# Performance work log

Measured on AMD Instinct MI355X. Metric: run time of the kernel, lower is better.

Reference implementation:

```python
import jax, jax.numpy as jnp
import numpy as np

B, S, H, NH = 2, 4096, 768, 12
DH = H // NH  # 64


def setup_inputs() -> dict:
    key = jax.random.key(0)
    ks = jax.random.split(key, 7)
    scale = 0.02
    return {
        "x": jax.random.normal(ks[0], (B, S, H), dtype=jnp.float32),
        "Wq": jax.random.normal(ks[1], (H, H), dtype=jnp.float32) * scale,
        "bq": jax.random.normal(ks[2], (H,), dtype=jnp.float32) * scale,
        "Wk": jax.random.normal(ks[3], (H, H), dtype=jnp.float32) * scale,
        "bk": jax.random.normal(ks[4], (H,), dtype=jnp.float32) * scale,
        "Wv": jax.random.normal(ks[5], (H, H), dtype=jnp.float32) * scale,
        "bv": jax.random.normal(ks[6], (H,), dtype=jnp.float32) * scale,
    }


def _split_heads(t):
    # [B,S,H] -> [B,NH,S,DH]
    return t.reshape(B, S, NH, DH).transpose(0, 2, 1, 3)


def reference(x, Wq, bq, Wk, bk, Wv, bv):
    q = _split_heads(x @ Wq + bq)
    k = _split_heads(x @ Wk + bk)
    v = _split_heads(x @ Wv + bv)
    # raw scores + zero additive mask (mask is all zeros, so it is a no-op)
    scores = jnp.einsum("bhqd,bhkd->bhqk", q, k) / jnp.sqrt(jnp.float32(DH))
    probs = jax.nn.softmax(scores, axis=-1)
    ctx = jnp.einsum("bhqk,bhkd->bhqd", probs, v)
    out = ctx.transpose(0, 2, 1, 3).reshape(B, S, H)
    return jnp.tanh(out)
```

## Files before the change

kernel.cpp:

```cpp
#include <hip/hip_runtime.h>
#include <hip/hip_bf16.h>

#define B_ 2
#define S_ 4096
#define H_ 768
#define NH_ 12
#define DH_ 64
#define M_ (B_ * S_)
#define N3_ (3 * H_)
#define NQK 1536
#define K_ H_
#define LOG2E 1.4426950408889634f

typedef __attribute__((ext_vector_type(8))) short short8;
typedef __attribute__((ext_vector_type(4))) float f32x4;
typedef __attribute__((ext_vector_type(16))) float f32x16;
typedef __attribute__((ext_vector_type(4))) unsigned int uint4v;
typedef __attribute__((ext_vector_type(4))) unsigned short ushort4v;

__device__ __forceinline__ unsigned short f2bf(float f) {
    unsigned int u = __builtin_bit_cast(unsigned int, f);
    u += 0x7FFFu + ((u >> 16) & 1u);
    return (unsigned short)(u >> 16);
}
__device__ __forceinline__ unsigned int cvtpk_bf16(float lo, float hi) {
    unsigned int r;
    asm("v_cvt_pk_bf16_f32 %0, %1, %2" : "=v"(r) : "v"(lo), "v"(hi));
    return r;
}
__device__ __forceinline__ void plswap32(unsigned int &x, unsigned int &y) {
    asm("v_permlane32_swap_b32 %0, %1" : "+v"(x), "+v"(y));
}
__device__ __forceinline__ float exp2_fast(float x) {
    float r;
    asm("v_exp_f32 %0, %1" : "=v"(r) : "v"(x));
    return r;
}

__global__ __launch_bounds__(256) void cast_w_kernel(const float* __restrict__ Wq,
                                                     const float* __restrict__ Wk,
                                                     const float* __restrict__ Wv,
                                                     unsigned short* __restrict__ wt) {
    int idx = blockIdx.x * 256 + threadIdx.x;
    int k = idx % H_;
    int nn = idx / H_;
    int n = nn % H_;
    int wsel = nn / H_;
    const float* W = (wsel == 0) ? Wq : (wsel == 1) ? Wk : Wv;
    wt[idx] = f2bf(W[k * H_ + n]);
}

#define BM 128
#define BN 128
#define BK 32
#define LDT 40

__global__ __launch_bounds__(256) void qkv_gemm_kernel(const float* __restrict__ x,
                                                       const unsigned short* __restrict__ wt,
                                                       const float* __restrict__ bq,
                                                       const float* __restrict__ bk,
                                                       const float* __restrict__ bv,
                                                       unsigned short* __restrict__ qk,
                                                       unsigned short* __restrict__ vT) {
    __shared__ unsigned short Asm[BM * LDT];
    __shared__ unsigned short Bsm[BN * LDT];
    const int tid = threadIdx.x;
    const int nTiles = N3_ / BN;
    const int bm = blockIdx.x / nTiles;
    const int bn = blockIdx.x % nTiles;
    const int w = tid >> 6, l = tid & 63;
    const int wm = w >> 1, wn = w & 1;
    const int lr = l & 15, lk = l >> 4;

    f32x4 zero = {0.f, 0.f, 0.f, 0.f};
    f32x4 acc[4][4];
#pragma unroll
    for (int i = 0; i < 4; i++)
#pragma unroll
        for (int j = 0; j < 4; j++) acc[i][j] = zero;

    const int srow = tid >> 2;
    const int scol = (tid & 3) * 8;
    const float* aG = x + (size_t)(bm * BM + srow) * K_ + scol;
    const unsigned short* bG = wt + (size_t)(bn * BN + srow) * K_ + scol;

    for (int k0 = 0; k0 < K_; k0 += BK) {
        __syncthreads();
#pragma unroll
        for (int half = 0; half < 2; half++) {
            float4 a0 = *reinterpret_cast<const float4*>(aG + (size_t)half * 64 * K_ + k0);
            float4 a1 = *reinterpret_cast<const float4*>(aG + (size_t)half * 64 * K_ + k0 + 4);
            union { unsigned short s[8]; uint4v v; } u;
            u.s[0] = f2bf(a0.x); u.s[1] = f2bf(a0.y); u.s[2] = f2bf(a0.z); u.s[3] = f2bf(a0.w);
            u.s[4] = f2bf(a1.x); u.s[5] = f2bf(a1.y); u.s[6] = f2bf(a1.z); u.s[7] = f2bf(a1.w);
            *reinterpret_cast<uint4v*>(&Asm[(srow + half * 64) * LDT + scol]) = u.v;
        }
        *reinterpret_cast<uint4v*>(&Bsm[srow * LDT + scol]) =
            *reinterpret_cast<const uint4v*>(bG + k0);
        *reinterpret_cast<uint4v*>(&Bsm[(srow + 64) * LDT + scol]) =
            *reinterpret_cast<const uint4v*>(bG + (size_t)64 * K_ + k0);
        __syncthreads();

        short8 a[4], b[4];
#pragma unroll
        for (int mi = 0; mi < 4; mi++)
            a[mi] = *reinterpret_cast<const short8*>(&Asm[(wm * 64 + mi * 16 + lr) * LDT + lk * 8]);
#pragma unroll
        for (int ni = 0; ni < 4; ni++)
            b[ni] = *reinterpret_cast<const short8*>(&Bsm[(wn * 64 + ni * 16 + lr) * LDT + lk * 8]);
#pragma unroll
        for (int mi = 0; mi < 4; mi++)
#pragma unroll
            for (int ni = 0; ni < 4; ni++)
                acc[mi][ni] = __builtin_amdgcn_mfma_f32_16x16x32_bf16(a[mi], b[ni], acc[mi][ni], 0, 0, 0);
    }

    if (bn < 12) {
#pragma unroll
        for (int ni = 0; ni < 4; ni++) {
            const int col = bn * BN + wn * 64 + ni * 16 + lr;
            const float bias = (col < H_) ? bq[col] : bk[col - H_];
#pragma unroll
            for (int mi = 0; mi < 4; mi++) {
#pragma unroll
                for (int i = 0; i < 4; i++) {
                    const int row = bm * BM + wm * 64 + mi * 16 + lk * 4 + i;
                    qk[(size_t)row * NQK + col] = f2bf(acc[mi][ni][i] + bias);
                }
            }
        }
    } else {
#pragma unroll
        for (int ni = 0; ni < 4; ni++) {
            const int c = bn * BN - 2 * H_ + wn * 64 + ni * 16 + lr;
            const int h = c >> 6, d = c & 63;
            const float bias = bv[c];
#pragma unroll
            for (int mi = 0; mi < 4; mi++) {
                const int row0 = bm * BM + wm * 64 + mi * 16 + lk * 4;
                const int b = row0 >> 12, s0 = row0 & (S_ - 1);
                union { unsigned short s[4]; ushort4v v; } u;
#pragma unroll
                for (int i = 0; i < 4; i++) u.s[i] = f2bf(acc[mi][ni][i] + bias);
                *reinterpret_cast<ushort4v*>(vT + ((size_t)(b * NH_ + h) * DH_ + d) * S_ + s0) = u.v;
            }
        }
    }
}

#define QW 32
#define QB 128
#define KB 64

__global__ __launch_bounds__(256, 2) void attn_kernel(const unsigned short* __restrict__ qk,
                                                      const unsigned short* __restrict__ vT,
                                                      float* __restrict__ out) {
    __shared__ unsigned short Ksm[KB * 64];
    __shared__ unsigned short Vsm[DH_ * KB];
    const int tid = threadIdx.x;
    const int w = tid >> 6, l = tid & 63;
    const int ln = l & 31, hi = l >> 5;
    const int swz = (blockIdx.x & 7) * 96 + (blockIdx.x >> 3);
    const int qt = swz & 31, bh = swz >> 5;
    const int b = bh / NH_, h = bh % NH_;

    const unsigned short* Qg = qk + (size_t)b * S_ * NQK + h * DH_;
    const unsigned short* Kg = Qg + H_;
    const unsigned short* Vg = vT + (size_t)bh * DH_ * S_;

    const int qrow = qt * QB + w * QW + ln;
    short8 qf[4];
    {
        const unsigned short* qp = Qg + (size_t)qrow * NQK + hi * 8;
#pragma unroll
        for (int dk = 0; dk < 4; dk++)
            qf[dk] = *reinterpret_cast<const short8*>(qp + dk * 16);
    }

    const f32x16 fz = {0,0,0,0,0,0,0,0,0,0,0,0,0,0,0,0};
    f32x16 o0 = fz, o1 = fz;
    float m_ = -INFINITY, lsum = 0.f;
    const float SCL = 0.125f * LOG2E;

    const int srow = tid >> 2;
    const int sd = (tid & 3) * 16;
    const unsigned short* kgp = Kg + (size_t)srow * NQK + sd;
    const unsigned short* vgp = Vg + (size_t)srow * S_ + sd;
    const int sidx0 = (srow * 64 + sd) ^ ((srow & 7) << 3);
    const int sidx1 = (srow * 64 + sd + 8) ^ ((srow & 7) << 3);

    for (int kt = 0; kt < S_; kt += KB) {
        __syncthreads();
        *reinterpret_cast<uint4v*>(&Ksm[sidx0]) = *reinterpret_cast<const uint4v*>(kgp + (size_t)kt * NQK);
        *reinterpret_cast<uint4v*>(&Ksm[sidx1]) = *reinterpret_cast<const uint4v*>(kgp + (size_t)kt * NQK + 8);
        *reinterpret_cast<uint4v*>(&Vsm[sidx0]) = *reinterpret_cast<const uint4v*>(vgp + kt);
        *reinterpret_cast<uint4v*>(&Vsm[sidx1]) = *reinterpret_cast<const uint4v*>(vgp + kt + 8);
        __syncthreads();

        f32x16 s0 = fz, s1 = fz;
#pragma unroll
        for (int dk = 0; dk < 4; dk++) {
            const int col = dk * 16 + hi * 8;
            short8 kf0 = *reinterpret_cast<const short8*>(&Ksm[(ln * 64 + col) ^ ((ln & 7) << 3)]);
            short8 kf1 = *reinterpret_cast<const short8*>(&Ksm[((32 + ln) * 64 + col) ^ ((ln & 7) << 3)]);
            s0 = __builtin_amdgcn_mfma_f32_32x32x16_bf16(kf0, qf[dk], s0, 0, 0, 0);
            s1 = __builtin_amdgcn_mfma_f32_32x32x16_bf16(kf1, qf[dk], s1, 0, 0, 0);
        }
#pragma unroll
        for (int r = 0; r < 16; r++) { s0[r] *= SCL; s1[r] *= SCL; }

        float pmax = s0[0];
#pragma unroll
        for (int r = 1; r < 16; r++) pmax = fmaxf(pmax, s0[r]);
#pragma unroll
        for (int r = 0; r < 16; r++) pmax = fmaxf(pmax, s1[r]);
        pmax = fmaxf(pmax, __shfl_xor(pmax, 32));
        if (!__all(pmax - m_ <= 8.0f)) {
            const float mnew = fmaxf(m_, pmax);
            const float corr = exp2_fast(m_ - mnew);
            m_ = mnew;
            lsum *= corr;
#pragma unroll
            for (int r = 0; r < 16; r++) {
                const float c = __shfl(corr, (r & 3) + 8 * (r >> 2) + 4 * hi);
                o0[r] *= c; o1[r] *= c;
            }
        }
        float p[32];
        float rs = 0.f;
#pragma unroll
        for (int r = 0; r < 16; r++) { p[r] = exp2_fast(s0[r] - m_); rs += p[r]; }
#pragma unroll
        for (int r = 0; r < 16; r++) { p[16 + r] = exp2_fast(s1[r] - m_); rs += p[16 + r]; }
        rs += __shfl_xor(rs, 32);
        lsum += rs;

        short8 pa[4];
#pragma unroll
        for (int half = 0; half < 2; half++) {
            unsigned int c0 = cvtpk_bf16(p[half*16+0],  p[half*16+1]);
            unsigned int c1 = cvtpk_bf16(p[half*16+2],  p[half*16+3]);
            unsigned int c2 = cvtpk_bf16(p[half*16+4],  p[half*16+5]);
            unsigned int c3 = cvtpk_bf16(p[half*16+6],  p[half*16+7]);
            unsigned int c4 = cvtpk_bf16(p[half*16+8],  p[half*16+9]);
            unsigned int c5 = cvtpk_bf16(p[half*16+10], p[half*16+11]);
            unsigned int c6 = cvtpk_bf16(p[half*16+12], p[half*16+13]);
            unsigned int c7 = cvtpk_bf16(p[half*16+14], p[half*16+15]);
            plswap32(c0, c2); plswap32(c1, c3);
            plswap32(c4, c6); plswap32(c5, c7);
            union { unsigned int u[4]; short8 v; } ua, ub;
            ua.u[0] = c0; ua.u[1] = c1; ua.u[2] = c2; ua.u[3] = c3;
            ub.u[0] = c4; ub.u[1] = c5; ub.u[2] = c6; ub.u[3] = c7;
            pa[half * 2]     = ua.v;
            pa[half * 2 + 1] = ub.v;
        }

#pragma unroll
        for (int s4 = 0; s4 < 4; s4++) {
            const int kcol = s4 * 16 + hi * 8;
            short8 vf0 = *reinterpret_cast<const short8*>(&Vsm[(ln * 64 + kcol) ^ ((ln & 7) << 3)]);
            short8 vf1 = *reinterpret_cast<const short8*>(&Vsm[((32 + ln) * 64 + kcol) ^ ((ln & 7) << 3)]);
            o0 = __builtin_amdgcn_mfma_f32_32x32x16_bf16(pa[s4], vf0, o0, 0, 0, 0);
            o1 = __builtin_amdgcn_mfma_f32_32x32x16_bf16(pa[s4], vf1, o1, 0, 0, 0);
        }
    }

    float* op = out + ((size_t)b * S_ + qt * QB + w * QW) * H_ + h * DH_;
#pragma unroll
    for (int r = 0; r < 16; r++) {
        const int q = (r & 3) + 8 * (r >> 2) + 4 * hi;
        const float inv = 1.0f / __shfl(lsum, q);
        op[(size_t)q * H_ + ln]      = tanhf(o0[r] * inv);
        op[(size_t)q * H_ + 32 + ln] = tanhf(o1[r] * inv);
    }
}

extern "C" void kernel_launch(void* const* d_in, const int* in_sizes, int n_in,
                              void* d_out, int out_size, void* d_ws, size_t ws_size,
                              hipStream_t stream) {
    const float* x  = (const float*)d_in[0];
    const float* Wq = (const float*)d_in[1];
    const float* bq = (const float*)d_in[2];
    const float* Wk = (const float*)d_in[3];
    const float* bk = (const float*)d_in[4];
    const float* Wv = (const float*)d_in[5];
    const float* bv = (const float*)d_in[6];
    float* out = (float*)d_out;

    char* ws = (char*)d_ws;
    unsigned short* wt = (unsigned short*)ws;
    size_t off = (size_t)N3_ * K_ * 2;
    unsigned short* qkb = (unsigned short*)(ws + off);
    off += (size_t)M_ * NQK * 2;
    unsigned short* vTb = (unsigned short*)(ws + off);

    cast_w_kernel<<<dim3((3 * H_ * H_) / 256), dim3(256), 0, stream>>>(Wq, Wk, Wv, wt);
    qkv_gemm_kernel<<<dim3((M_ / BM) * (N3_ / BN)), dim3(256), 0, stream>>>(x, wt, bq, bk, bv, qkb, vTb);
    attn_kernel<<<dim3(B_ * NH_ * (S_ / QB)), dim3(256), 0, stream>>>(qkb, vTb, out);
}
```

Before: 321.8 us.

## Pre-cast x, use direct global-to-LDS GEMM loads, prefetch K/V, fold softmax scale

Adds a separate kernel that casts x to bf16 and vectorises the weight transpose-cast. The QKV GEMM now loads with global_load_lds at BK=64, uses an XCD-aware block swizzle, and drops padded LDS. The attention kernel register-prefetches the next K/V tile before the barrier, and the softmax scale is folded into Q at GEMM time, removing a per-tile multiply. The extra cast kernel adds a full read and write of x, and the unpadded LDS layout in the GEMM may cause bank conflicts.

```diff
diff --git a/kernel.cpp b/kernel.cpp
--- a/kernel.cpp
+++ b/kernel.cpp
@@ -18,6 +18,9 @@
 typedef __attribute__((ext_vector_type(4))) unsigned int uint4v;
 typedef __attribute__((ext_vector_type(4))) unsigned short ushort4v;
 
+typedef __attribute__((address_space(3))) unsigned int lds_u32;
+typedef const __attribute__((address_space(1))) unsigned int glb_u32;
+
 __device__ __forceinline__ unsigned short f2bf(float f) {
     unsigned int u = __builtin_bit_cast(unsigned int, f);
     u += 0x7FFFu + ((u >> 16) & 1u);
@@ -37,37 +40,46 @@
     return r;
 }
 
+__global__ __launch_bounds__(256) void cast_x_kernel(const float* __restrict__ x,
+                                                     unsigned short* __restrict__ xb) {
+    int i = blockIdx.x * 256 + threadIdx.x;
+    float4 v = reinterpret_cast<const float4*>(x)[i];
+    ushort4 o;
+    o.x = f2bf(v.x); o.y = f2bf(v.y); o.z = f2bf(v.z); o.w = f2bf(v.w);
+    reinterpret_cast<ushort4*>(xb)[i] = o;
+}
+
 __global__ __launch_bounds__(256) void cast_w_kernel(const float* __restrict__ Wq,
                                                      const float* __restrict__ Wk,
                                                      const float* __restrict__ Wv,
                                                      unsigned short* __restrict__ wt) {
-    int idx = blockIdx.x * 256 + threadIdx.x;
-    int k = idx % H_;
-    int nn = idx / H_;
-    int n = nn % H_;
-    int wsel = nn / H_;
+    int id = blockIdx.x * 256 + threadIdx.x;
+    int n = id % H_;
+    int kb = (id / H_) % 96;
+    int wsel = id / (H_ * 96);
     const float* W = (wsel == 0) ? Wq : (wsel == 1) ? Wk : Wv;
-    wt[idx] = f2bf(W[k * H_ + n]);
-}
-
-#define BM 128
-#define BN 128
-#define BK 32
-#define LDT 40
-
-__global__ __launch_bounds__(256) void qkv_gemm_kernel(const float* __restrict__ x,
+    union { unsigned short s[8]; uint4v v; } u;
+#pragma unroll
+    for (int j = 0; j < 8; j++) u.s[j] = f2bf(W[(size_t)(kb * 8 + j) * H_ + n]);
+    *reinterpret_cast<uint4v*>(wt + (size_t)(wsel * H_ + n) * H_ + kb * 8) = u.v;
+}
+
+#define GBM 128
+#define GBN 128
+#define GBK 64
+
+__global__ __launch_bounds__(256) void qkv_gemm_kernel(const unsigned short* __restrict__ xb,
                                                        const unsigned short* __restrict__ wt,
                                                        const float* __restrict__ bq,
                                                        const float* __restrict__ bk,
                                                        const float* __restrict__ bv,
                                                        unsigned short* __restrict__ qk,
                                                        unsigned short* __restrict__ vT) {
-    __shared__ unsigned short Asm[BM * LDT];
-    __shared__ unsigned short Bsm[BN * LDT];
+    __shared__ unsigned short Asm[GBM * GBK];
+    __shared__ unsigned short Bsm[GBN * GBK];
     const int tid = threadIdx.x;
-    const int nTiles = N3_ / BN;
-    const int bm = blockIdx.x / nTiles;
-    const int bn = blockIdx.x % nTiles;
+    const int swz = (blockIdx.x & 7) * 144 + (blockIdx.x >> 3);
+    const int bm = swz / 18, bn = swz % 18;
     const int w = tid >> 6, l = tid & 63;
     const int wm = w >> 1, wn = w & 1;
     const int lr = l & 15, lk = l >> 4;
@@ -79,65 +91,71 @@
 #pragma unroll
         for (int j = 0; j < 4; j++) acc[i][j] = zero;
 
-    const int srow = tid >> 2;
-    const int scol = (tid & 3) * 8;
-    const float* aG = x + (size_t)(bm * BM + srow) * K_ + scol;
-    const unsigned short* bG = wt + (size_t)(bn * BN + srow) * K_ + scol;
-
-    for (int k0 = 0; k0 < K_; k0 += BK) {
+    const int srow = l >> 3;
+    const int scol = (l & 7) * 8;
+    const unsigned short* aBase = xb + (size_t)(bm * GBM) * K_;
+    const unsigned short* bBase = wt + (size_t)(bn * GBN) * K_;
+
+    for (int k0 = 0; k0 < K_; k0 += GBK) {
         __syncthreads();
 #pragma unroll
-        for (int half = 0; half < 2; half++) {
-            float4 a0 = *reinterpret_cast<const float4*>(aG + (size_t)half * 64 * K_ + k0);
-            float4 a1 = *reinterpret_cast<const float4*>(aG + (size_t)half * 64 * K_ + k0 + 4);
-            union { unsigned short s[8]; uint4v v; } u;
-            u.s[0] = f2bf(a0.x); u.s[1] = f2bf(a0.y); u.s[2] = f2bf(a0.z); u.s[3] = f2bf(a0.w);
-            u.s[4] = f2bf(a1.x); u.s[5] = f2bf(a1.y); u.s[6] = f2bf(a1.z); u.s[7] = f2bf(a1.w);
-            *reinterpret_cast<uint4v*>(&Asm[(srow + half * 64) * LDT + scol]) = u.v;
-        }
-        *reinterpret_cast<uint4v*>(&Bsm[srow * LDT + scol]) =
-            *reinterpret_cast<const uint4v*>(bG + k0);
-        *reinterpret_cast<uint4v*>(&Bsm[(srow + 64) * LDT + scol]) =
-            *reinterpret_cast<const uint4v*>(bG + (size_t)64 * K_ + k0);
+        for (int i = 0; i < 4; i++) {
+            const int j = w * 4 + i;
+            __builtin_amdgcn_global_load_lds(
+                (glb_u32*)(aBase + (size_t)(j * 8 + srow) * K_ + k0 + scol),
+                (lds_u32*)(&Asm[j * 8 * GBK]), 16, 0, 0);
+        }
+#pragma unroll
+        for (int i = 0; i < 4; i++) {
+            const int j = w * 4 + i;
+            __builtin_amdgcn_global_load_lds(
+                (glb_u32*)(bBase + (size_t)(j * 8 + srow) * K_ + k0 + scol),
+                (lds_u32*)(&Bsm[j * 8 * GBK]), 16, 0, 0);
+        }
         __syncthreads();
 
-        short8 a[4], b[4];
-#pragma unroll
-        for (int mi = 0; mi < 4; mi++)
-            a[mi] = *reinterpret_cast<const short8*>(&Asm[(wm * 64 + mi * 16 + lr) * LDT + lk * 8]);
-#pragma unroll
-        for (int ni = 0; ni < 4; ni++)
-            b[ni] = *reinterpret_cast<const short8*>(&Bsm[(wn * 64 + ni * 16 + lr) * LDT + lk * 8]);
-#pragma unroll
-        for (int mi = 0; mi < 4; mi++)
+#pragma unroll
+        for (int ks = 0; ks < 2; ks++) {
+            short8 a[4], b[4];
+#pragma unroll
+            for (int mi = 0; mi < 4; mi++)
+                a[mi] = *reinterpret_cast<const short8*>(&Asm[(wm * 64 + mi * 16 + lr) * GBK + ks * 32 + lk * 8]);
 #pragma unroll
             for (int ni = 0; ni < 4; ni++)
-                acc[mi][ni] = __builtin_amdgcn_mfma_f32_16x16x32_bf16(a[mi], b[ni], acc[mi][ni], 0, 0, 0);
+                b[ni] = *reinterpret_cast<const short8*>(&Bsm[(wn * 64 + ni * 16 + lr) * GBK + ks * 32 + lk * 8]);
+#pragma unroll
+            for (int mi = 0; mi < 4; mi++)
+#pragma unroll
+                for (int ni = 0; ni < 4; ni++)
+                    acc[mi][ni] = __builtin_amdgcn_mfma_f32_16x16x32_bf16(a[mi], b[ni], acc[mi][ni], 0, 0, 0);
+        }
     }
 
     if (bn < 12) {
 #pragma unroll
         for (int ni = 0; ni < 4; ni++) {
-            const int col = bn * BN + wn * 64 + ni * 16 + lr;
-            const float bias = (col < H_) ? bq[col] : bk[col - H_];
+            const int col = bn * GBN + wn * 64 + ni * 16 + lr;
+            const bool isQ = (col < H_);
+            const float bias = isQ ? bq[col] : bk[col - H_];
+            const float scl = isQ ? (0.125f * LOG2E) : 1.0f;
 #pragma unroll
             for (int mi = 0; mi < 4; mi++) {
 #pragma unroll
                 for (int i = 0; i < 4; i++) {
-                    const int row = bm * BM + wm * 64 + mi * 16 + lk * 4 + i;
-                    qk[(size_t)row * NQK + col] = f2bf(acc[mi][ni][i] + bias);
+                    const int row = bm * GBM + wm * 64 + mi * 16 + lk * 4 + i;
+                    qk[(size_t)row * NQK + col] = f2bf((acc[mi][ni][i] + bias) * scl);
                 }
             }
         }
     } else {
 #pragma unroll
         for (int ni = 0; ni < 4; ni++) {
-            const int c = bn * BN - 2 * H_ + wn * 64 + ni * 16 + lr;
+            const int c = bn * GBN - 2 * H_ + wn * 64 + ni * 16 + lr;
             const int h = c >> 6, d = c & 63;
             const float bias = bv[c];
 #pragma unroll
             for (int mi = 0; mi < 4; mi++) {
-                const int row0 = bm * BM + wm * 64 + mi * 16 + lk * 4;
+                const int row0 = bm * GBM + wm * 64 + mi * 16 + lk * 4;
                 const int b = row0 >> 12, s0 = row0 & (S_ - 1);
                 union { unsigned short s[4]; ushort4v v; } u;
 #pragma unroll
@@ -180,7 +198,6 @@
     const f32x16 fz = {0,0,0,0,0,0,0,0,0,0,0,0,0,0,0,0};
     f32x16 o0 = fz, o1 = fz;
     float m_ = -INFINITY, lsum = 0.f;
-    const float SCL = 0.125f * LOG2E;
 
     const int srow = tid >> 2;
     const int sd = (tid & 3) * 16;
@@ -189,13 +206,28 @@
     const int sidx0 = (srow * 64 + sd) ^ ((srow & 7) << 3);
     const int sidx1 = (srow * 64 + sd + 8) ^ ((srow & 7) << 3);
 
+    uint4v kr0 = *reinterpret_cast<const uint4v*>(kgp);
+    uint4v kr1 = *reinterpret_cast<const uint4v*>(kgp + 8);
+    uint4v vr0 = *reinterpret_cast<const uint4v*>(vgp);
+    uint4v vr1 = *reinterpret_cast<const uint4v*>(vgp + 8);
+
     for (int kt = 0; kt < S_; kt += KB) {
-        __syncthreads();
-        *reinterpret_cast<uint4v*>(&Ksm[sidx0]) = *reinterpret_cast<const uint4v*>(kgp + (size_t)kt * NQK);
-        *reinterpret_cast<uint4v*>(&Ksm[sidx1]) = *reinterpret_cast<const uint4v*>(kgp + (size_t)kt * NQK + 8);
-        *reinterpret_cast<uint4v*>(&Vsm[sidx0]) = *reinterpret_cast<const uint4v*>(vgp + kt);
-        *reinterpret_cast<uint4v*>(&Vsm[sidx1]) = *reinterpret_cast<const uint4v*>(vgp + kt + 8);
-        __syncthreads();
+        asm volatile("" ::: "memory");
+        __builtin_amdgcn_s_barrier();
+        asm volatile("" ::: "memory");
+        *reinterpret_cast<uint4v*>(&Ksm[sidx0]) = kr0;
+        *reinterpret_cast<uint4v*>(&Ksm[sidx1]) = kr1;
+        *reinterpret_cast<uint4v*>(&Vsm[sidx0]) = vr0;
+        *reinterpret_cast<uint4v*>(&Vsm[sidx1]) = vr1;
+        if (kt + KB < S_) {
+            kr0 = *reinterpret_cast<const uint4v*>(kgp + (size_t)(kt + KB) * NQK);
+            kr1 = *reinterpret_cast<const uint4v*>(kgp + (size_t)(kt + KB) * NQK + 8);
+            vr0 = *reinterpret_cast<const uint4v*>(vgp + kt + KB);
+            vr1 = *reinterpret_cast<const uint4v*>(vgp + kt + KB + 8);
+        }
+        asm volatile("s_waitcnt lgkmcnt(0)" ::: "memory");
+        __builtin_amdgcn_s_barrier();
+        asm volatile("" ::: "memory");
 
         f32x16 s0 = fz, s1 = fz;
 #pragma unroll
@@ -206,14 +238,14 @@
             s0 = __builtin_amdgcn_mfma_f32_32x32x16_bf16(kf0, qf[dk], s0, 0, 0, 0);
             s1 = __builtin_amdgcn_mfma_f32_32x32x16_bf16(kf1, qf[dk], s1, 0, 0, 0);
         }
-#pragma unroll
-        for (int r = 0; r < 16; r++) { s0[r] *= SCL; s1[r] *= SCL; }
-
-        float pmax = s0[0];
-#pragma unroll
-        for (int r = 1; r < 16; r++) pmax = fmaxf(pmax, s0[r]);
-#pragma unroll
-        for (int r = 0; r < 16; r++) pmax = fmaxf(pmax, s1[r]);
+
+        float pmax = fmaxf(fmaxf(s0[0], s0[1]), fmaxf(s0[2], s0[3]));
+#pragma unroll
+        for (int r = 4; r < 16; r += 4)
+            pmax = fmaxf(pmax, fmaxf(fmaxf(s0[r], s0[r+1]), fmaxf(s0[r+2], s0[r+3])));
+#pragma unroll
+        for (int r = 0; r < 16; r += 4)
+            pmax = fmaxf(pmax, fmaxf(fmaxf(s1[r], s1[r+1]), fmaxf(s1[r+2], s1[r+3])));
         pmax = fmaxf(pmax, __shfl_xor(pmax, 32));
         if (!__all(pmax - m_ <= 8.0f)) {
             const float mnew = fmaxf(m_, pmax);
@@ -288,13 +320,16 @@
     float* out = (float*)d_out;
 
     char* ws = (char*)d_ws;
-    unsigned short* wt = (unsigned short*)ws;
-    size_t off = (size_t)N3_ * K_ * 2;
+    unsigned short* xb = (unsigned short*)ws;
+    size_t off = (size_t)M_ * K_ * 2;
+    unsigned short* wt = (unsigned short*)(ws + off);
+    off += (size_t)N3_ * K_ * 2;
     unsigned short* qkb = (unsigned short*)(ws + off);
     off += (size_t)M_ * NQK * 2;
     unsigned short* vTb = (unsigned short*)(ws + off);
 
-    cast_w_kernel<<<dim3((3 * H_ * H_) / 256), dim3(256), 0, stream>>>(Wq, Wk, Wv, wt);
-    qkv_gemm_kernel<<<dim3((M_ / BM) * (N3_ / BN)), dim3(256), 0, stream>>>(x, wt, bq, bk, bv, qkb, vTb);
+    cast_x_kernel<<<dim3((M_ * K_) / 4 / 256), dim3(256), 0, stream>>>(x, xb);
+    cast_w_kernel<<<dim3((3 * H_ * 96) / 256), dim3(256), 0, stream>>>(Wq, Wk, Wv, wt);
+    qkv_gemm_kernel<<<dim3((M_ / GBM) * (N3_ / GBN)), dim3(256), 0, stream>>>(xb, wt, bq, bk, bv, qkb, vTb);
     attn_kernel<<<dim3(B_ * NH_ * (S_ / QB)), dim3(256), 0, stream>>>(qkb, vTb, out);
 }
```

Measured after the change: 284.3 us. 11.7% less time.
